# Performance work log

Hardware: AMD Instinct MI355X
Metric: run time of the kernel (lower is better)

Reference implementation:

```python
import jax, jax.numpy as jnp
import numpy as np

R = 0.2          # radius of the continuous kernel support
N_RINGS = 4      # radial ring basis functions
C_IN = 32        # input feature channels (coords concatenated -> 35)
C_OUT = 64       # output channels
FIELD_DIM = 4    # channels per field for the norm nonlinearity (16 fields)
N_PTS = 32768
M_PTS = 8192
N_EDGES = M_PTS * 64  # max_num_neighbors=64 per sampled center


def setup_inputs() -> dict:
    key = jax.random.key(0)
    ks = jax.random.split(key, 9)
    x = jax.random.normal(ks[0], (N_PTS, C_IN), dtype=jnp.float32)
    pos = jax.random.uniform(ks[1], (N_PTS, 3), dtype=jnp.float32)
    # fps stand-in: random subset of centers; radius stand-in: random candidate
    # neighbors, the r-ball constraint is enforced by the dist<=R mask in the kernel
    idx = jax.random.randint(ks[2], (M_PTS,), 0, N_PTS)
    edge_src = jax.random.randint(ks[3], (N_EDGES,), 0, N_PTS)
    edge_dst = jax.random.randint(ks[4], (N_EDGES,), 0, M_PTS)
    # learned params: ring weights for the continuous kernel, BN affine, norm-nl bias
    W = jax.random.normal(ks[5], (N_RINGS, C_OUT, C_IN + 3), dtype=jnp.float32) * 0.1
    gamma = jnp.ones((C_OUT,), dtype=jnp.float32)
    beta = jnp.zeros((C_OUT,), dtype=jnp.float32)
    nbias = jax.random.normal(ks[6], (C_OUT // FIELD_DIM,), dtype=jnp.float32) * 0.1
    return {"x": x, "pos": pos, "idx": idx, "edge_src": edge_src,
            "edge_dst": edge_dst, "W": W, "gamma": gamma, "beta": beta,
            "nbias": nbias}


def reference(x, pos, idx, edge_src, edge_dst, W, gamma, beta, nbias):
    M = idx.shape[0]
    # concat coords to features (first_conv is None branch)
    h = jnp.concatenate([x, pos], axis=1)                      # [N, Cin+3]
    pos_out = pos[idx]                                          # [M, 3]
    # per-edge relative geometry (gather)
    rel = pos[edge_src] - pos_out[edge_dst]                     # [E, 3]
    dist = jnp.sqrt(jnp.sum(rel * rel, axis=1) + 1e-12)        # [E]
    # radial ring basis with hard radius cutoff
    centers = jnp.linspace(0.0, R, N_RINGS, dtype=dist.dtype)
    sigma = R / N_RINGS
    valid = (dist <= R).astype(dist.dtype)                     # [E]
    basis = jnp.exp(-0.5 * ((dist[:, None] - centers) / sigma) ** 2) * valid[:, None]
    # continuous-kernel point conv: per-edge kernel @ gathered features
    msg = jnp.einsum('ek,koi,ei->eo', basis, W, h[edge_src])   # [E, Cout]
    # scatter-mean aggregation to sampled centers
    agg = jax.ops.segment_sum(msg, edge_dst, num_segments=M)   # [M, Cout]
    cnt = jax.ops.segment_sum(valid, edge_dst, num_segments=M)
    a = agg / jnp.maximum(cnt, 1.0)[:, None]
    # IID batch norm (training-mode batch stats over points)
    mu = jnp.mean(a, axis=0)
    var = jnp.var(a, axis=0)
    y = (a - mu) * jax.lax.rsqrt(var + 1e-5) * gamma + beta
    # norm nonlinearity: scale each field's vector by elu(norm + bias)/norm
    v = y.reshape(M, C_OUT // FIELD_DIM, FIELD_DIM)
    n = jnp.sqrt(jnp.sum(v * v, axis=-1, keepdims=True) + 1e-12)
    out = v * (jax.nn.elu(n + nbias[None, :, None]) / n)
    return out.reshape(M, C_OUT)
```

## Files before the change

kernel.cpp:

```cpp
#include <hip/hip_runtime.h>
#include <math.h>

#define N_PTS_C 32768
#define M_PTS_C 8192
#define EDGES_C (M_PTS_C * 64)
#define CH 35
#define COUT 64
#define NR 4
#define KI (NR * CH)
#define CAP 64
#define RCUT 0.2f
#define SIG_INV 20.0f


__global__ __launch_bounds__(256) void k_edge(
    const float* __restrict__ pos, const int* __restrict__ idx,
    const int* __restrict__ esrc, const int* __restrict__ edst,
    int* __restrict__ cnt, int2* __restrict__ rec)
{
    int e = blockIdx.x * 256 + threadIdx.x;
    int src = esrc[e];
    int dst = edst[e];
    int cpt = idx[dst];
    float dx = pos[src*3+0] - pos[cpt*3+0];
    float dy = pos[src*3+1] - pos[cpt*3+1];
    float dz = pos[src*3+2] - pos[cpt*3+2];
    float dist = sqrtf(dx*dx + dy*dy + dz*dz + 1e-12f);
    if (dist <= RCUT) {
        int slot = atomicAdd(&cnt[dst], 1);
        if (slot < CAP) rec[dst*CAP + slot] = make_int2(src, __float_as_int(dist));
    }
}

__global__ __launch_bounds__(256) void k_center(
    const float* __restrict__ x, const float* __restrict__ pos,
    const float* __restrict__ W, const int* __restrict__ cnt,
    const int2* __restrict__ rec, float* __restrict__ aout)
{
    __shared__ float Wl[KI * COUT];
    __shared__ float Fl[16][KI];
    __shared__ int   nvl[16];

    int tid = threadIdx.x;
    for (int t = tid; t < KI * COUT; t += 256) Wl[t] = W[t];

    int m0 = blockIdx.x * 16;
    int c = tid >> 4;
    int lane = tid & 15;
    int m = m0 + c;
    int nv = min(cnt[m], CAP);
    if (lane == 0) nvl[c] = nv;

    float facc[9];
    #pragma unroll
    for (int u = 0; u < 9; ++u) facc[u] = 0.f;

    for (int j = 0; j < nv; ++j) {
        int2 r = rec[m*CAP + j];
        int src = r.x;
        float dist = __int_as_float(r.y);
        float t0 = dist * SIG_INV;
        float t1 = (dist - (float)(0.2/3.0)) * SIG_INV;
        float t2 = (dist - (float)(0.4/3.0)) * SIG_INV;
        float t3 = (dist - 0.2f) * SIG_INV;
        float b0 = expf(-0.5f*t0*t0);
        float b1 = expf(-0.5f*t1*t1);
        float b2 = expf(-0.5f*t2*t2);
        float b3 = expf(-0.5f*t3*t3);
        #pragma unroll
        for (int u = 0; u < 9; ++u) {
            int ki = lane + u*16;
            if (ki < KI) {
                int k = ki / CH;
                int i = ki - k*CH;
                float hv = (i < 32) ? x[src*32 + i] : pos[src*3 + (i - 32)];
                float bk = (k==0) ? b0 : (k==1) ? b1 : (k==2) ? b2 : b3;
                facc[u] += bk * hv;
            }
        }
    }
    #pragma unroll
    for (int u = 0; u < 9; ++u) {
        int ki = lane + u*16;
        if (ki < KI) Fl[c][ki] = facc[u];
    }
    __syncthreads();

    int o = tid & 63;
    int g = tid >> 6;
    #pragma unroll 1
    for (int r = 0; r < 4; ++r) {
        int cc = r*4 + g;
        float acc = 0.f;
        #pragma unroll
        for (int k = 0; k < NR; ++k) {
            const float* wrow = &Wl[(k*COUT + o)*CH];
            const float* frow = &Fl[cc][k*CH];
            #pragma unroll
            for (int i = 0; i < CH; ++i) acc += wrow[i] * frow[i];
        }
        float nvf = (float)nvl[cc];
        aout[(m0 + cc)*COUT + o] = acc / fmaxf(nvf, 1.f);
    }
}

__global__ __launch_bounds__(256) void k_bn(
    const float* __restrict__ a, float* __restrict__ mu, float* __restrict__ rs)
{
    int o = blockIdx.x, t = threadIdx.x;
    float s = 0.f, q = 0.f;
    for (int m = t; m < M_PTS_C; m += 256) {
        float v = a[m*COUT + o];
        s += v; q += v*v;
    }
    __shared__ float ss[256], sq[256];
    ss[t] = s; sq[t] = q;
    __syncthreads();
    for (int w = 128; w >= 1; w >>= 1) {
        if (t < w) { ss[t] += ss[t+w]; sq[t] += sq[t+w]; }
        __syncthreads();
    }
    if (t == 0) {
        float m_ = ss[0] * (1.f / M_PTS_C);
        float v_ = sq[0] * (1.f / M_PTS_C) - m_*m_;
        mu[o] = m_;
        rs[o] = rsqrtf(v_ + 1e-5f);
    }
}

__global__ __launch_bounds__(256) void k_post(
    const float* __restrict__ a, const float* __restrict__ mu,
    const float* __restrict__ rs, const float* __restrict__ gamma,
    const float* __restrict__ beta, const float* __restrict__ nbias,
    float* __restrict__ out)
{
    int flat = blockIdx.x * 256 + threadIdx.x;
    int f = flat & 15;
    const float4* a4 = (const float4*)a;
    float4 v = a4[flat];
    float y[4];
    float nn = 1e-12f;
    #pragma unroll
    for (int jj = 0; jj < 4; ++jj) {
        int o = f*4 + jj;
        float val = (jj==0) ? v.x : (jj==1) ? v.y : (jj==2) ? v.z : v.w;
        float yy = (val - mu[o]) * rs[o] * gamma[o] + beta[o];
        y[jj] = yy;
        nn += yy*yy;
    }
    float n = sqrtf(nn);
    float z = n + nbias[f];
    float e = (z > 0.f) ? z : expm1f(z);
    float sc = e / n;
    float4 ov;
    ov.x = y[0]*sc; ov.y = y[1]*sc; ov.z = y[2]*sc; ov.w = y[3]*sc;
    ((float4*)out)[flat] = ov;
}

extern "C" void kernel_launch(void* const* d_in, const int* in_sizes, int n_in,
                              void* d_out, int out_size, void* d_ws, size_t ws_size,
                              hipStream_t stream)
{
    const float* x     = (const float*)d_in[0];
    const float* pos   = (const float*)d_in[1];
    const int*   idx   = (const int*)d_in[2];
    const int*   esrc  = (const int*)d_in[3];
    const int*   edst  = (const int*)d_in[4];
    const float* W     = (const float*)d_in[5];
    const float* gamma = (const float*)d_in[6];
    const float* beta  = (const float*)d_in[7];
    const float* nbias = (const float*)d_in[8];

    char* ws = (char*)d_ws;
    int*   cnt = (int*)ws;
    float* mu  = (float*)(ws + 32768);
    float* rsg = (float*)(ws + 33024);
    int2*  rec = (int2*)(ws + 33280);
    float* a   = (float*)(ws + 4227584);

    hipMemsetAsync(cnt, 0, 32768, stream);
    k_edge<<<EDGES_C/256, 256, 0, stream>>>(pos, idx, esrc, edst, cnt, rec);
    k_center<<<M_PTS_C/16, 256, 0, stream>>>(x, pos, W, cnt, rec, a);
    k_bn<<<COUT, 256, 0, stream>>>(a, mu, rsg);
    k_post<<<(M_PTS_C*16)/256, 256, 0, stream>>>(a, mu, rsg, gamma, beta, nbias, (float*)d_out);
}
```

Before: 120.8 us.

## Fuse all stages into one persistent cooperative kernel with grid syncs

Merges the memset, edge filter, center conv, batch-norm stats and post nonlinearity into a single cooperative kernel whose phases are separated by grid-wide syncs. It also precomputes center positions into a compact buffer. The aim is to remove several kernel launch gaps and the memset call. In exchange the grid is limited to occupancy-sized persistent blocks, the BN phase uses only 64 blocks while the rest idle, and the large shared memory footprint bounds occupancy. There is a fallback to separate launches if the cooperative launch fails.

```diff
diff --git a/kernel.cpp b/kernel.cpp
--- a/kernel.cpp
+++ b/kernel.cpp
@@ -1,5 +1,8 @@
 #include <hip/hip_runtime.h>
+#include <hip/hip_cooperative_groups.h>
 #include <math.h>
+
+namespace cg = cooperative_groups;
 
 #define N_PTS_C 32768
 #define M_PTS_C 8192
@@ -13,148 +16,153 @@
 #define SIG_INV 20.0f
 
 
-__global__ __launch_bounds__(256) void k_edge(
-    const float* __restrict__ pos, const int* __restrict__ idx,
-    const int* __restrict__ esrc, const int* __restrict__ edst,
-    int* __restrict__ cnt, int2* __restrict__ rec)
-{
-    int e = blockIdx.x * 256 + threadIdx.x;
-    int src = esrc[e];
-    int dst = edst[e];
-    int cpt = idx[dst];
-    float dx = pos[src*3+0] - pos[cpt*3+0];
-    float dy = pos[src*3+1] - pos[cpt*3+1];
-    float dz = pos[src*3+2] - pos[cpt*3+2];
-    float dist = sqrtf(dx*dx + dy*dy + dz*dz + 1e-12f);
-    if (dist <= RCUT) {
-        int slot = atomicAdd(&cnt[dst], 1);
-        if (slot < CAP) rec[dst*CAP + slot] = make_int2(src, __float_as_int(dist));
-    }
-}
-
-__global__ __launch_bounds__(256) void k_center(
+__global__ __launch_bounds__(256, 3) void k_all(
     const float* __restrict__ x, const float* __restrict__ pos,
-    const float* __restrict__ W, const int* __restrict__ cnt,
-    const int2* __restrict__ rec, float* __restrict__ aout)
+    const int* __restrict__ idx, const int* __restrict__ esrc,
+    const int* __restrict__ edst, const float* __restrict__ W,
+    const float* __restrict__ gamma, const float* __restrict__ beta,
+    const float* __restrict__ nbias,
+    int* __restrict__ cnt, float* __restrict__ pos_c,
+    float* __restrict__ mu, float* __restrict__ rs,
+    int2* __restrict__ rec, float* __restrict__ a, float* __restrict__ out,
+    int p_lo, int p_hi, int coop)
 {
     __shared__ float Wl[KI * COUT];
     __shared__ float Fl[16][KI];
     __shared__ int   nvl[16];
-
+    __shared__ float ss[256], sq[256];
+
+    cg::grid_group gg = cg::this_grid();
     int tid = threadIdx.x;
-    for (int t = tid; t < KI * COUT; t += 256) Wl[t] = W[t];
-
-    int m0 = blockIdx.x * 16;
-    int c = tid >> 4;
-    int lane = tid & 15;
-    int m = m0 + c;
-    int nv = min(cnt[m], CAP);
-    if (lane == 0) nvl[c] = nv;
-
-    float facc[9];
-    #pragma unroll
-    for (int u = 0; u < 9; ++u) facc[u] = 0.f;
-
-    for (int j = 0; j < nv; ++j) {
-        int2 r = rec[m*CAP + j];
-        int src = r.x;
-        float dist = __int_as_float(r.y);
-        float t0 = dist * SIG_INV;
-        float t1 = (dist - (float)(0.2/3.0)) * SIG_INV;
-        float t2 = (dist - (float)(0.4/3.0)) * SIG_INV;
-        float t3 = (dist - 0.2f) * SIG_INV;
-        float b0 = expf(-0.5f*t0*t0);
-        float b1 = expf(-0.5f*t1*t1);
-        float b2 = expf(-0.5f*t2*t2);
-        float b3 = expf(-0.5f*t3*t3);
-        #pragma unroll
-        for (int u = 0; u < 9; ++u) {
-            int ki = lane + u*16;
-            if (ki < KI) {
-                int k = ki / CH;
-                int i = ki - k*CH;
-                float hv = (i < 32) ? x[src*32 + i] : pos[src*3 + (i - 32)];
-                float bk = (k==0) ? b0 : (k==1) ? b1 : (k==2) ? b2 : b3;
-                facc[u] += bk * hv;
+    int gtid = blockIdx.x * 256 + tid;
+    int gsz = gridDim.x * 256;
+
+    for (int p = p_lo; p <= p_hi; ++p) {
+        if (p == 0) {
+            for (int m = gtid; m < M_PTS_C; m += gsz) {
+                cnt[m] = 0;
+                int c = idx[m];
+                pos_c[m*3+0] = pos[c*3+0];
+                pos_c[m*3+1] = pos[c*3+1];
+                pos_c[m*3+2] = pos[c*3+2];
+            }
+        } else if (p == 1) {
+            for (int e = gtid; e < EDGES_C; e += gsz) {
+                int src = esrc[e];
+                int dst = edst[e];
+                float dx = pos[src*3+0] - pos_c[dst*3+0];
+                float dy = pos[src*3+1] - pos_c[dst*3+1];
+                float dz = pos[src*3+2] - pos_c[dst*3+2];
+                float dist = sqrtf(dx*dx + dy*dy + dz*dz + 1e-12f);
+                if (dist <= RCUT) {
+                    int slot = atomicAdd(&cnt[dst], 1);
+                    if (slot < CAP) rec[dst*CAP + slot] = make_int2(src, __float_as_int(dist));
+                }
+            }
+        } else if (p == 2) {
+            for (int t = tid; t < (KI*COUT)/4; t += 256)
+                ((float4*)Wl)[t] = ((const float4*)W)[t];
+            for (int grp = blockIdx.x; grp < M_PTS_C/16; grp += gridDim.x) {
+                __syncthreads();
+                int c = tid >> 4, lane = tid & 15;
+                int m = grp*16 + c;
+                int nv = min(cnt[m], CAP);
+                if (lane == 0) nvl[c] = nv;
+                float facc[9];
+                #pragma unroll
+                for (int u = 0; u < 9; ++u) facc[u] = 0.f;
+                for (int j = 0; j < nv; ++j) {
+                    int2 r = rec[m*CAP + j];
+                    int src = r.x;
+                    float dist = __int_as_float(r.y);
+                    float t0 = dist * SIG_INV;
+                    float t1 = (dist - (float)(0.2/3.0)) * SIG_INV;
+                    float t2 = (dist - (float)(0.4/3.0)) * SIG_INV;
+                    float t3 = (dist - 0.2f) * SIG_INV;
+                    float b0 = expf(-0.5f*t0*t0);
+                    float b1 = expf(-0.5f*t1*t1);
+                    float b2 = expf(-0.5f*t2*t2);
+                    float b3 = expf(-0.5f*t3*t3);
+                    #pragma unroll
+                    for (int u = 0; u < 9; ++u) {
+                        int ki = lane + u*16;
+                        if (ki < KI) {
+                            int k = ki / CH;
+                            int i = ki - k*CH;
+                            float hv = (i < 32) ? x[src*32 + i] : pos[src*3 + (i - 32)];
+                            float bk = (k==0) ? b0 : (k==1) ? b1 : (k==2) ? b2 : b3;
+                            facc[u] += bk * hv;
+                        }
+                    }
+                }
+                #pragma unroll
+                for (int u = 0; u < 9; ++u) {
+                    int ki = lane + u*16;
+                    if (ki < KI) Fl[c][ki] = facc[u];
+                }
+                __syncthreads();
+                int o = tid & 63, g = tid >> 6;
+                #pragma unroll 1
+                for (int r = 0; r < 4; ++r) {
+                    int cc = r*4 + g;
+                    float acc = 0.f;
+                    #pragma unroll
+                    for (int k = 0; k < NR; ++k) {
+                        const float* wrow = &Wl[(k*COUT + o)*CH];
+                        const float* frow = &Fl[cc][k*CH];
+                        #pragma unroll
+                        for (int i = 0; i < CH; ++i) acc += wrow[i] * frow[i];
+                    }
+                    float nvf = (float)nvl[cc];
+                    a[(grp*16 + cc)*COUT + o] = acc / fmaxf(nvf, 1.f);
+                }
+            }
+        } else if (p == 3) {
+            for (int o = blockIdx.x; o < COUT; o += gridDim.x) {
+                float s = 0.f, q = 0.f;
+                for (int m = tid; m < M_PTS_C; m += 256) {
+                    float v = a[m*COUT + o];
+                    s += v; q += v*v;
+                }
+                ss[tid] = s; sq[tid] = q;
+                __syncthreads();
+                for (int w = 128; w >= 1; w >>= 1) {
+                    if (tid < w) { ss[tid] += ss[tid+w]; sq[tid] += sq[tid+w]; }
+                    __syncthreads();
+                }
+                if (tid == 0) {
+                    float m_ = ss[0] * (1.f / M_PTS_C);
+                    float v_ = sq[0] * (1.f / M_PTS_C) - m_*m_;
+                    mu[o] = m_;
+                    rs[o] = rsqrtf(v_ + 1e-5f);
+                }
+                __syncthreads();
+            }
+        } else if (p == 4) {
+            for (int flat = gtid; flat < M_PTS_C*16; flat += gsz) {
+                int f = flat & 15;
+                float4 v = ((const float4*)a)[flat];
+                float y[4];
+                float nn = 1e-12f;
+                #pragma unroll
+                for (int jj = 0; jj < 4; ++jj) {
+                    int o = f*4 + jj;
+                    float val = (jj==0) ? v.x : (jj==1) ? v.y : (jj==2) ? v.z : v.w;
+                    float yy = (val - mu[o]) * rs[o] * gamma[o] + beta[o];
+                    y[jj] = yy;
+                    nn += yy*yy;
+                }
+                float n = sqrtf(nn);
+                float z = n + nbias[f];
+                float e = (z > 0.f) ? z : expm1f(z);
+                float sc = e / n;
+                float4 ov;
+                ov.x = y[0]*sc; ov.y = y[1]*sc; ov.z = y[2]*sc; ov.w = y[3]*sc;
+                ((float4*)out)[flat] = ov;
             }
         }
+        if (p < p_hi && coop) gg.sync();
     }
-    #pragma unroll
-    for (int u = 0; u < 9; ++u) {
-        int ki = lane + u*16;
-        if (ki < KI) Fl[c][ki] = facc[u];
-    }
-    __syncthreads();
-
-    int o = tid & 63;
-    int g = tid >> 6;
-    #pragma unroll 1
-    for (int r = 0; r < 4; ++r) {
-        int cc = r*4 + g;
-        float acc = 0.f;
-        #pragma unroll
-        for (int k = 0; k < NR; ++k) {
-            const float* wrow = &Wl[(k*COUT + o)*CH];
-            const float* frow = &Fl[cc][k*CH];
-            #pragma unroll
-            for (int i = 0; i < CH; ++i) acc += wrow[i] * frow[i];
-        }
-        float nvf = (float)nvl[cc];
-        aout[(m0 + cc)*COUT + o] = acc / fmaxf(nvf, 1.f);
-    }
-}
-
-__global__ __launch_bounds__(256) void k_bn(
-    const float* __restrict__ a, float* __restrict__ mu, float* __restrict__ rs)
-{
-    int o = blockIdx.x, t = threadIdx.x;
-    float s = 0.f, q = 0.f;
-    for (int m = t; m < M_PTS_C; m += 256) {
-        float v = a[m*COUT + o];
-        s += v; q += v*v;
-    }
-    __shared__ float ss[256], sq[256];
-    ss[t] = s; sq[t] = q;
-    __syncthreads();
-    for (int w = 128; w >= 1; w >>= 1) {
-        if (t < w) { ss[t] += ss[t+w]; sq[t] += sq[t+w]; }
-        __syncthreads();
-    }
-    if (t == 0) {
-        float m_ = ss[0] * (1.f / M_PTS_C);
-        float v_ = sq[0] * (1.f / M_PTS_C) - m_*m_;
-        mu[o] = m_;
-        rs[o] = rsqrtf(v_ + 1e-5f);
-    }
-}
-
-__global__ __launch_bounds__(256) void k_post(
-    const float* __restrict__ a, const float* __restrict__ mu,
-    const float* __restrict__ rs, const float* __restrict__ gamma,
-    const float* __restrict__ beta, const float* __restrict__ nbias,
-    float* __restrict__ out)
-{
-    int flat = blockIdx.x * 256 + threadIdx.x;
-    int f = flat & 15;
-    const float4* a4 = (const float4*)a;
-    float4 v = a4[flat];
-    float y[4];
-    float nn = 1e-12f;
-    #pragma unroll
-    for (int jj = 0; jj < 4; ++jj) {
-        int o = f*4 + jj;
-        float val = (jj==0) ? v.x : (jj==1) ? v.y : (jj==2) ? v.z : v.w;
-        float yy = (val - mu[o]) * rs[o] * gamma[o] + beta[o];
-        y[jj] = yy;
-        nn += yy*yy;
-    }
-    float n = sqrtf(nn);
-    float z = n + nbias[f];
-    float e = (z > 0.f) ? z : expm1f(z);
-    float sc = e / n;
-    float4 ov;
-    ov.x = y[0]*sc; ov.y = y[1]*sc; ov.z = y[2]*sc; ov.w = y[3]*sc;
-    ((float4*)out)[flat] = ov;
 }
 
 extern "C" void kernel_launch(void* const* d_in, const int* in_sizes, int n_in,
@@ -172,15 +180,34 @@
     const float* nbias = (const float*)d_in[8];
 
     char* ws = (char*)d_ws;
-    int*   cnt = (int*)ws;
-    float* mu  = (float*)(ws + 32768);
-    float* rsg = (float*)(ws + 33024);
-    int2*  rec = (int2*)(ws + 33280);
-    float* a   = (float*)(ws + 4227584);
-
-    hipMemsetAsync(cnt, 0, 32768, stream);
-    k_edge<<<EDGES_C/256, 256, 0, stream>>>(pos, idx, esrc, edst, cnt, rec);
-    k_center<<<M_PTS_C/16, 256, 0, stream>>>(x, pos, W, cnt, rec, a);
-    k_bn<<<COUT, 256, 0, stream>>>(a, mu, rsg);
-    k_post<<<(M_PTS_C*16)/256, 256, 0, stream>>>(a, mu, rsg, gamma, beta, nbias, (float*)d_out);
+    int*   cnt   = (int*)ws;
+    float* pos_c = (float*)(ws + 32768);
+    float* mu    = (float*)(ws + 131072);
+    float* rs    = (float*)(ws + 131328);
+    int2*  rec   = (int2*)(ws + 131584);
+    float* a     = (float*)(ws + 4325888);
+    float* outp  = (float*)d_out;
+
+    int occ = 0;
+    hipError_t oe = hipOccupancyMaxActiveBlocksPerMultiprocessor(&occ, k_all, 256, 0);
+    if (oe != hipSuccess || occ < 1) occ = 1;
+    int grid = occ * 256;
+
+    int plo = 0, phi = 4, coop = 1;
+    void* args[] = {
+        (void*)&x, (void*)&pos, (void*)&idx, (void*)&esrc, (void*)&edst,
+        (void*)&W, (void*)&gamma, (void*)&beta, (void*)&nbias,
+        (void*)&cnt, (void*)&pos_c, (void*)&mu, (void*)&rs,
+        (void*)&rec, (void*)&a, (void*)&outp,
+        (void*)&plo, (void*)&phi, (void*)&coop
+    };
+    hipError_t le = hipLaunchCooperativeKernel(k_all, dim3(grid), dim3(256),
+                                               args, 0, stream);
+    if (le != hipSuccess) {
+        k_all<<<32,   256, 0, stream>>>(x,pos,idx,esrc,edst,W,gamma,beta,nbias,cnt,pos_c,mu,rs,rec,a,outp,0,0,0);
+        k_all<<<2048, 256, 0, stream>>>(x,pos,idx,esrc,edst,W,gamma,beta,nbias,cnt,pos_c,mu,rs,rec,a,outp,1,1,0);
+        k_all<<<512,  256, 0, stream>>>(x,pos,idx,esrc,edst,W,gamma,beta,nbias,cnt,pos_c,mu,rs,rec,a,outp,2,2,0);
+        k_all<<<64,   256, 0, stream>>>(x,pos,idx,esrc,edst,W,gamma,beta,nbias,cnt,pos_c,mu,rs,rec,a,outp,3,3,0);
+        k_all<<<512,  256, 0, stream>>>(x,pos,idx,esrc,edst,W,gamma,beta,nbias,cnt,pos_c,mu,rs,rec,a,outp,4,4,0);
+    }
 }
```

After: 341.2 us. 183% more time.

## Fuse BN statistics into center kernel and pack positions as float4

Applied to the files above, without the earlier changes.

Replaces the memset with an init kernel that zeroes counters and stat sums and builds padded float4 copies of point and center positions. The edge kernel then does single float4 gathers and handles two edges per thread with vectorized index loads. The separate batch-norm reduction kernel is removed: the center kernel accumulates per-channel sum and sum-of-squares and atomically adds them to global, and the post kernel derives mean and rstd into shared memory. This saves a launch and a pass over the aggregate, at the cost of float atomic ordering nondeterminism in the stats.

```diff
diff --git a/kernel.cpp b/kernel.cpp
--- a/kernel.cpp
+++ b/kernel.cpp
@@ -13,36 +13,65 @@
 #define SIG_INV 20.0f
 
 
+__global__ __launch_bounds__(256) void k_init(
+    const float* __restrict__ pos, const int* __restrict__ idx,
+    int* __restrict__ cnt, float* __restrict__ sums,
+    float4* __restrict__ pos_c4, float4* __restrict__ pos4)
+{
+    int gtid = blockIdx.x * 256 + threadIdx.x;
+    int gsz = gridDim.x * 256;
+    for (int n = gtid; n < N_PTS_C; n += gsz) {
+        float4 p;
+        p.x = pos[n*3+0]; p.y = pos[n*3+1]; p.z = pos[n*3+2]; p.w = 0.f;
+        pos4[n] = p;
+    }
+    for (int m = gtid; m < M_PTS_C; m += gsz) {
+        cnt[m] = 0;
+        int c = idx[m];
+        float4 p;
+        p.x = pos[c*3+0]; p.y = pos[c*3+1]; p.z = pos[c*3+2]; p.w = 0.f;
+        pos_c4[m] = p;
+    }
+    if (gtid < 128) sums[gtid] = 0.f;
+}
+
 __global__ __launch_bounds__(256) void k_edge(
-    const float* __restrict__ pos, const int* __restrict__ idx,
+    const float4* __restrict__ pos4, const float4* __restrict__ pos_c4,
     const int* __restrict__ esrc, const int* __restrict__ edst,
     int* __restrict__ cnt, int2* __restrict__ rec)
 {
-    int e = blockIdx.x * 256 + threadIdx.x;
-    int src = esrc[e];
-    int dst = edst[e];
-    int cpt = idx[dst];
-    float dx = pos[src*3+0] - pos[cpt*3+0];
-    float dy = pos[src*3+1] - pos[cpt*3+1];
-    float dz = pos[src*3+2] - pos[cpt*3+2];
-    float dist = sqrtf(dx*dx + dy*dy + dz*dz + 1e-12f);
-    if (dist <= RCUT) {
-        int slot = atomicAdd(&cnt[dst], 1);
-        if (slot < CAP) rec[dst*CAP + slot] = make_int2(src, __float_as_int(dist));
+    int t = blockIdx.x * 256 + threadIdx.x;
+    int2 s2 = ((const int2*)esrc)[t];
+    int2 d2 = ((const int2*)edst)[t];
+    #pragma unroll
+    for (int q = 0; q < 2; ++q) {
+        int src = (q == 0) ? s2.x : s2.y;
+        int dst = (q == 0) ? d2.x : d2.y;
+        float4 ps = pos4[src];
+        float4 pc = pos_c4[dst];
+        float dx = ps.x - pc.x, dy = ps.y - pc.y, dz = ps.z - pc.z;
+        float dist = sqrtf(dx*dx + dy*dy + dz*dz + 1e-12f);
+        if (dist <= RCUT) {
+            int slot = atomicAdd(&cnt[dst], 1);
+            if (slot < CAP) rec[dst*CAP + slot] = make_int2(src, __float_as_int(dist));
+        }
     }
 }
 
 __global__ __launch_bounds__(256) void k_center(
     const float* __restrict__ x, const float* __restrict__ pos,
     const float* __restrict__ W, const int* __restrict__ cnt,
-    const int2* __restrict__ rec, float* __restrict__ aout)
+    const int2* __restrict__ rec, float* __restrict__ aout,
+    float* __restrict__ sums)
 {
     __shared__ float Wl[KI * COUT];
     __shared__ float Fl[16][KI];
     __shared__ int   nvl[16];
+    __shared__ float ss[256], sq[256];
 
     int tid = threadIdx.x;
-    for (int t = tid; t < KI * COUT; t += 256) Wl[t] = W[t];
+    for (int t = tid; t < (KI*COUT)/4; t += 256)
+        ((float4*)Wl)[t] = ((const float4*)W)[t];
 
     int m0 = blockIdx.x * 16;
     int c = tid >> 4;
@@ -86,8 +115,8 @@
     }
     __syncthreads();
 
-    int o = tid & 63;
-    int g = tid >> 6;
+    int o = tid & 63, g = tid >> 6;
+    float psum = 0.f, psq = 0.f;
     #pragma unroll 1
     for (int r = 0; r < 4; ++r) {
         int cc = r*4 + g;
@@ -100,51 +129,50 @@
             for (int i = 0; i < CH; ++i) acc += wrow[i] * frow[i];
         }
         float nvf = (float)nvl[cc];
-        aout[(m0 + cc)*COUT + o] = acc / fmaxf(nvf, 1.f);
-    }
-}
-
-__global__ __launch_bounds__(256) void k_bn(
-    const float* __restrict__ a, float* __restrict__ mu, float* __restrict__ rs)
-{
-    int o = blockIdx.x, t = threadIdx.x;
-    float s = 0.f, q = 0.f;
-    for (int m = t; m < M_PTS_C; m += 256) {
-        float v = a[m*COUT + o];
-        s += v; q += v*v;
-    }
-    __shared__ float ss[256], sq[256];
-    ss[t] = s; sq[t] = q;
+        float av = acc / fmaxf(nvf, 1.f);
+        aout[(m0 + cc)*COUT + o] = av;
+        psum += av;
+        psq  += av*av;
+    }
+    ss[tid] = psum; sq[tid] = psq;
     __syncthreads();
-    for (int w = 128; w >= 1; w >>= 1) {
-        if (t < w) { ss[t] += ss[t+w]; sq[t] += sq[t+w]; }
-        __syncthreads();
-    }
-    if (t == 0) {
-        float m_ = ss[0] * (1.f / M_PTS_C);
-        float v_ = sq[0] * (1.f / M_PTS_C) - m_*m_;
-        mu[o] = m_;
-        rs[o] = rsqrtf(v_ + 1e-5f);
+    if (tid < 64) {
+        float s = ss[tid] + ss[tid+64] + ss[tid+128] + ss[tid+192];
+        float q = sq[tid] + sq[tid+64] + sq[tid+128] + sq[tid+192];
+        atomicAdd(&sums[tid], s);
+        atomicAdd(&sums[64 + tid], q);
     }
 }
 
 __global__ __launch_bounds__(256) void k_post(
-    const float* __restrict__ a, const float* __restrict__ mu,
-    const float* __restrict__ rs, const float* __restrict__ gamma,
-    const float* __restrict__ beta, const float* __restrict__ nbias,
-    float* __restrict__ out)
-{
-    int flat = blockIdx.x * 256 + threadIdx.x;
+    const float* __restrict__ a, const float* __restrict__ sums,
+    const float* __restrict__ gamma, const float* __restrict__ beta,
+    const float* __restrict__ nbias, float* __restrict__ out)
+{
+    __shared__ float smu[64], srs[64], sg[64], sb[64];
+    int tid = threadIdx.x;
+    if (tid < 64) {
+        float s = sums[tid];
+        float q = sums[64 + tid];
+        float m_ = s * (1.f / M_PTS_C);
+        float v_ = q * (1.f / M_PTS_C) - m_*m_;
+        smu[tid] = m_;
+        srs[tid] = rsqrtf(v_ + 1e-5f);
+        sg[tid] = gamma[tid];
+        sb[tid] = beta[tid];
+    }
+    __syncthreads();
+
+    int flat = blockIdx.x * 256 + tid;
     int f = flat & 15;
-    const float4* a4 = (const float4*)a;
-    float4 v = a4[flat];
+    float4 v = ((const float4*)a)[flat];
     float y[4];
     float nn = 1e-12f;
     #pragma unroll
     for (int jj = 0; jj < 4; ++jj) {
         int o = f*4 + jj;
         float val = (jj==0) ? v.x : (jj==1) ? v.y : (jj==2) ? v.z : v.w;
-        float yy = (val - mu[o]) * rs[o] * gamma[o] + beta[o];
+        float yy = (val - smu[o]) * srs[o] * sg[o] + sb[o];
         y[jj] = yy;
         nn += yy*yy;
     }
@@ -172,15 +200,15 @@
     const float* nbias = (const float*)d_in[8];
 
     char* ws = (char*)d_ws;
-    int*   cnt = (int*)ws;
-    float* mu  = (float*)(ws + 32768);
-    float* rsg = (float*)(ws + 33024);
-    int2*  rec = (int2*)(ws + 33280);
-    float* a   = (float*)(ws + 4227584);
-
-    hipMemsetAsync(cnt, 0, 32768, stream);
-    k_edge<<<EDGES_C/256, 256, 0, stream>>>(pos, idx, esrc, edst, cnt, rec);
-    k_center<<<M_PTS_C/16, 256, 0, stream>>>(x, pos, W, cnt, rec, a);
-    k_bn<<<COUT, 256, 0, stream>>>(a, mu, rsg);
-    k_post<<<(M_PTS_C*16)/256, 256, 0, stream>>>(a, mu, rsg, gamma, beta, nbias, (float*)d_out);
-}
+    int*    cnt    = (int*)ws;
+    float*  sums   = (float*)(ws + 32768);
+    float4* pos_c4 = (float4*)(ws + 33280);
+    float4* pos4   = (float4*)(ws + 164352);
+    int2*   rec    = (int2*)(ws + 688640);
+    float*  a      = (float*)(ws + 4882944);
+
+    k_init<<<128, 256, 0, stream>>>(pos, idx, cnt, sums, pos_c4, pos4);
+    k_edge<<<EDGES_C/512, 256, 0, stream>>>(pos4, pos_c4, esrc, edst, cnt, rec);
+    k_center<<<M_PTS_C/16, 256, 0, stream>>>(x, pos, W, cnt, rec, a, sums);
+    k_post<<<(M_PTS_C*16)/256, 256, 0, stream>>>(a, sums, gamma, beta, nbias, (float*)d_out);
+}
```

Result: faster. 109.0 us (-9.8%).
